# Kernel optimization log

Hardware: AMD Instinct MI355X
Metric: run time of the kernel (lower is better)

Reference implementation:

```python
import jax, jax.numpy as jnp
import numpy as np

NEG_SLOPE = 0.2  # PyG GATConv default leaky_relu slope


def gat_conv(x, edge_index, W, a_src, a_dst, b):
    """PyG GATConv (heads=1, concat=True, add_self_loops=True, dropout=0)."""
    N = x.shape[0]
    loops = jnp.arange(N, dtype=edge_index.dtype)
    src = jnp.concatenate([edge_index[0], loops])  # [Ef]
    dst = jnp.concatenate([edge_index[1], loops])  # [Ef]
    h = x @ W  # [N, Dout]
    alpha_src = h @ a_src  # [N]
    alpha_dst = h @ a_dst  # [N]
    logits = jax.nn.leaky_relu(alpha_src[src] + alpha_dst[dst], NEG_SLOPE)  # [Ef]
    # segment softmax over edges grouped by destination node
    m = jax.ops.segment_max(logits, dst, num_segments=N)
    e = jnp.exp(logits - m[dst])
    denom = jax.ops.segment_sum(e, dst, num_segments=N)  # >0: every node has a self-loop
    alpha = e / denom[dst]  # [Ef]
    out = jax.ops.segment_sum(alpha[:, None] * h[src], dst, num_segments=N)
    return out + b


def global_mean_pool(x, batch, num_graphs):
    s = jax.ops.segment_sum(x, batch, num_segments=num_graphs)
    cnt = jax.ops.segment_sum(jnp.ones((x.shape[0],), x.dtype), batch, num_segments=num_graphs)
    return s / jnp.maximum(cnt, 1.0)[:, None]


NUM_GRAPHS = 64


def setup_inputs() -> dict:
    key = jax.random.key(0)
    ks = jax.random.split(key, 12)
    N, E, D = 50000, 600000, 128
    x = jax.random.normal(ks[0], (N, D), dtype=jnp.float32)
    edge_index = jax.random.randint(ks[1], (2, E), 0, N, dtype=jnp.int32)
    edge_weight = jax.random.uniform(ks[2], (E,), dtype=jnp.float32)
    batch = jnp.sort(jax.random.randint(ks[3], (N,), 0, NUM_GRAPHS, dtype=jnp.int32))
    sc = 1.0 / np.sqrt(D)
    W0 = jax.random.normal(ks[4], (D, D), dtype=jnp.float32) * sc
    a_src0 = jax.random.normal(ks[5], (D,), dtype=jnp.float32) * sc
    a_dst0 = jax.random.normal(ks[6], (D,), dtype=jnp.float32) * sc
    b0 = jnp.zeros((D,), dtype=jnp.float32)
    W1 = jax.random.normal(ks[7], (D, D), dtype=jnp.float32) * sc
    a_src1 = jax.random.normal(ks[8], (D,), dtype=jnp.float32) * sc
    a_dst1 = jax.random.normal(ks[9], (D,), dtype=jnp.float32) * sc
    b1 = jnp.zeros((D,), dtype=jnp.float32)
    return {"x": x, "edge_index": edge_index, "edge_weight": edge_weight, "batch": batch,
            "W0": W0, "a_src0": a_src0, "a_dst0": a_dst0, "b0": b0,
            "W1": W1, "a_src1": a_src1, "a_dst1": a_dst1, "b1": b1}


def reference(x, edge_index, edge_weight, batch, W0, a_src0, a_dst0, b0, W1, a_src1, a_dst1, b1):
    # layer 0 (relu_layers_index=[0] -> ReLU after layer 0)
    out = gat_conv(x, edge_index, W0, a_src0, a_dst0, b0)
    out = jax.nn.relu(out)
    emb0 = global_mean_pool(out, batch, NUM_GRAPHS)
    # layer 1 (no relu, no dropout)
    out = gat_conv(out, edge_index, W1, a_src1, a_dst1, b1)
    emb1 = global_mean_pool(out, batch, NUM_GRAPHS)
    return (emb0, emb1)
```

## Files before the change

kernel.cpp:

```cpp
#include <hip/hip_runtime.h>
#include <hip/hip_cooperative_groups.h>

typedef unsigned int u32;
typedef unsigned short u16;
typedef unsigned long long u64;

typedef short bf16x8 __attribute__((ext_vector_type(8)));
typedef float f32x4 __attribute__((ext_vector_type(4)));
typedef float f32x2 __attribute__((ext_vector_type(2)));

__device__ __forceinline__ float bl(u32 u){ return __uint_as_float(u << 16); }
__device__ __forceinline__ float bh(u32 u){ return __uint_as_float(u & 0xffff0000u); }
__device__ __forceinline__ float b16f(u16 r){ return __uint_as_float(((u32)r) << 16); }
__device__ __forceinline__ u16 f2b(float f){
  u32 u = __float_as_uint(f);
  u32 r = (u + 0x7fffu + ((u >> 16) & 1u)) >> 16;
  return (u16)r;
}
__device__ __forceinline__ u32 pk2(float a, float b){
  return (u32)f2b(a) | ((u32)f2b(b) << 16);
}
__device__ __forceinline__ void fma8(float* acc, float e2, uint2 h){
  f32x2 p0 = __builtin_amdgcn_cvt_pk_f32_fp8((int)h.x, 0);
  f32x2 p1 = __builtin_amdgcn_cvt_pk_f32_fp8((int)h.x, 1);
  f32x2 p2 = __builtin_amdgcn_cvt_pk_f32_fp8((int)h.y, 0);
  f32x2 p3 = __builtin_amdgcn_cvt_pk_f32_fp8((int)h.y, 1);
  acc[0]=fmaf(e2,p0.x,acc[0]); acc[1]=fmaf(e2,p0.y,acc[1]);
  acc[2]=fmaf(e2,p1.x,acc[2]); acc[3]=fmaf(e2,p1.y,acc[3]);
  acc[4]=fmaf(e2,p2.x,acc[4]); acc[5]=fmaf(e2,p2.y,acc[5]);
  acc[6]=fmaf(e2,p3.x,acc[6]); acc[7]=fmaf(e2,p3.y,acc[7]);
}

#define NEG_SLOPE 0.2f
#define BSTRIDE 4096
#define SMBYTES 34816



__device__ __forceinline__ int detect_body(const u32* __restrict__ x, char* SM){
  int* cnt_ = (int*)SM;
  if (threadIdx.x == 0) *cnt_ = 0;
  __syncthreads();
  u32 w = x[threadIdx.x];
  int e = (int)((w >> 7) & 0xFFu);
  if (e >= 110 && e <= 135) atomicAdd(cnt_, 1);
  __syncthreads();
  return (*cnt_ >= 128) ? 1 : 0;
}

__device__ __forceinline__ void bnd_body(const int* __restrict__ batch,
    int* __restrict__ bnd, int N)
{
  int g = threadIdx.x;
  if (g <= 64){
    int lo = 0, hi = N;
    while (lo < hi){ int mid = (lo + hi) >> 1; if (batch[mid] < g) lo = mid + 1; else hi = mid; }
    bnd[g] = lo;
  }
}

__device__ __forceinline__ void part_body(const int* __restrict__ ei, int E, int nbuck,
    int* __restrict__ gcnt, u64* __restrict__ breg, int job, char* SM)
{
  u64* stage = (u64*)SM;
  u32* hist  = (u32*)(SM + 16384);
  u32* lscan = (u32*)(SM + 17408);
  u32* gbase = (u32*)(SM + 18436);
  u32* cur   = (u32*)(SM + 19460);
  const int tid = threadIdx.x;
  __syncthreads();
  hist[tid] = 0; cur[tid] = 0;
  __syncthreads();
  const int e0 = job * 2048;
  int src[8], dst[8];
  #pragma unroll
  for (int j = 0; j < 8; j++){
    int t = e0 + tid + j*256;
    if (t < E){
      src[j] = ei[t]; dst[j] = ei[E + t];
      atomicAdd(&hist[dst[j] >> 8], 1u);
    } else dst[j] = -1;
  }
  __syncthreads();
  const u32 v = hist[tid];
  lscan[tid] = v;
  __syncthreads();
  for (int off = 1; off < 256; off <<= 1){
    u32 add = (tid >= off) ? lscan[tid - off] : 0;
    __syncthreads();
    lscan[tid] += add;
    __syncthreads();
  }
  if (tid == 255) lscan[256] = lscan[255];
  u32 excl = lscan[tid] - v;
  __syncthreads();
  const u32 total = lscan[256];
  lscan[tid] = excl;
  if (tid < nbuck && v > 0) gbase[tid] = (u32)atomicAdd(&gcnt[tid], (int)v);
  __syncthreads();
  #pragma unroll
  for (int j = 0; j < 8; j++){
    if (dst[j] >= 0){
      int b = dst[j] >> 8;
      u32 p = lscan[b] + atomicAdd(&cur[b], 1u);
      stage[p] = ((u64)(u32)dst[j] << 32) | (u32)src[j];
    }
  }
  __syncthreads();
  for (u32 i = tid; i < total; i += 256){
    u64 e = stage[i];
    int b = (int)(e >> 40);
    u32 r = i - lscan[b];
    breg[(long)b * BSTRIDE + gbase[b] + r] = e;
  }
}

__device__ __forceinline__ void csr_body(const int* __restrict__ gcnt,
    const u64* __restrict__ breg,
    int* __restrict__ rpd, int* __restrict__ csrc, int N, int job, char* SM)
{
  u32* dl = (u32*)SM;
  u32* rp = dl + 256;
  u32* cu = rp + 256;
  const int b = job, tid = threadIdx.x;
  const int n0 = b << 8;
  __syncthreads();
  const int cntb = gcnt[b];
  dl[tid] = 0; cu[tid] = 0;
  __syncthreads();
  const u64* reg = breg + (long)b * BSTRIDE;
  for (int i = tid; i < cntb; i += 256)
    atomicAdd(&dl[(int)(reg[i] >> 32) - n0], 1u);
  __syncthreads();
  const u32 v = dl[tid];
  rp[tid] = v;
  __syncthreads();
  for (int off = 1; off < 256; off <<= 1){
    u32 add = (tid >= off) ? rp[tid - off] : 0;
    __syncthreads();
    rp[tid] += add;
    __syncthreads();
  }
  u32 excl = rp[tid] - v;
  __syncthreads();
  rp[tid] = excl;
  __syncthreads();
  int node = n0 + tid;
  if (node < N) rpd[node] = (int)(((u32)(b*BSTRIDE) + excl) | (v << 20));
  for (int i = tid; i < cntb; i += 256){
    u64 e = reg[i];
    int d = (int)(e >> 32) - n0;
    u32 pos = rp[d] + atomicAdd(&cu[d], 1u);
    csrc[(long)b*BSTRIDE + pos] = (int)(e & 0xffffffffULL);
  }
}

template<bool XEXT, bool KPERM>
__device__ __forceinline__ void gemm_body(int gb, int isbf,
    const void* __restrict__ Xv, const void* __restrict__ Wv,
    const void* __restrict__ av, const void* __restrict__ dv,
    u32* __restrict__ Hb, float* __restrict__ As, float* __restrict__ Ad, int N, char* SM)
{
  u16* Wt = (u16*)SM;
  const int tid = threadIdx.x;
  __syncthreads();

  if (isbf){
    const u32* Wp = (const u32*)Wv;
    #pragma unroll
    for (int i = 0; i < 16; i++){
      int idx = tid + i*256;
      u32 p = Wp[idx];
      int k = idx >> 6, n2 = idx & 63;
      int pos = KPERM ? ((k & 15)*8 + (k >> 4)) : k;
      Wt[(2*n2)*136 + pos]   = (u16)(p & 0xffffu);
      Wt[(2*n2+1)*136 + pos] = (u16)(p >> 16);
    }
  } else {
    const float* Wf = (const float*)Wv;
    #pragma unroll
    for (int i = 0; i < 64; i++){
      int idx = tid + i*256;
      int k = idx >> 7, n = idx & 127;
      int pos = KPERM ? ((k & 15)*8 + (k >> 4)) : k;
      Wt[n*136 + pos] = f2b(Wf[idx]);
    }
  }
  __syncthreads();

  const int wv = tid >> 6, L = tid & 63;
  const int row0 = (gb*4 + wv) * 16;
  if (row0 >= N) return;
  const int nl = L & 15, quad = L >> 4;

  bf16x8 af[4];
  if (!XEXT || isbf){
    const uint4* Xr = (const uint4*)(((const u32*)Xv) + (long)row0*64);
    #pragma unroll
    for (int kb = 0; kb < 4; kb++)
      af[kb] = *(const bf16x8*)&Xr[nl*16 + kb*4 + quad];
  } else {
    const float* Xf = ((const float*)Xv) + (long)(row0 + nl)*128;
    #pragma unroll
    for (int kb = 0; kb < 4; kb++){
      const float4* p = (const float4*)(Xf + kb*32 + quad*8);
      float4 f0 = p[0], f1 = p[1];
      uint4 tmp = make_uint4(pk2(f0.x,f0.y), pk2(f0.z,f0.w), pk2(f1.x,f1.y), pk2(f1.z,f1.w));
      af[kb] = *(const bf16x8*)&tmp;
    }
  }

  f32x4 acc[8];
  #pragma unroll
  for (int nt = 0; nt < 8; nt++) acc[nt] = (f32x4){0.f,0.f,0.f,0.f};
  #pragma unroll
  for (int nt = 0; nt < 8; nt++){
    #pragma unroll
    for (int kb = 0; kb < 4; kb++){
      bf16x8 bf = *(const bf16x8*)&Wt[(nt*16 + nl)*136 + kb*32 + quad*8];
      acc[nt] = __builtin_amdgcn_mfma_f32_16x16x32_bf16(af[kb], bf, acc[nt], 0, 0, 0);
    }
  }

  float ps[4] = {0.f,0.f,0.f,0.f}, pd[4] = {0.f,0.f,0.f,0.f};
  #pragma unroll
  for (int nt = 0; nt < 8; nt++){
    int col = nt*16 + nl;
    float a_ = isbf ? b16f(((const u16*)av)[col]) : ((const float*)av)[col];
    float d_ = isbf ? b16f(((const u16*)dv)[col]) : ((const float*)dv)[col];
    #pragma unroll
    for (int r = 0; r < 4; r++){
      ps[r] = fmaf(acc[nt][r], a_, ps[r]);
      pd[r] = fmaf(acc[nt][r], d_, pd[r]);
    }
  }
  #pragma unroll
  for (int off = 1; off < 16; off <<= 1){
    #pragma unroll
    for (int r = 0; r < 4; r++){
      ps[r] += __shfl_xor(ps[r], off);
      pd[r] += __shfl_xor(pd[r], off);
    }
  }
  if (nl == 0){
    #pragma unroll
    for (int r = 0; r < 4; r++){
      As[row0 + quad*4 + r] = ps[r];
      Ad[row0 + quad*4 + r] = pd[r];
    }
  }

  #pragma unroll
  for (int r = 0; r < 4; r++){
    long row = row0 + quad*4 + r;
    int w0 = 0, w1 = 0;
    w0 = __builtin_amdgcn_cvt_pk_fp8_f32(acc[0][r], acc[1][r], w0, 0);
    w0 = __builtin_amdgcn_cvt_pk_fp8_f32(acc[2][r], acc[3][r], w0, 1);
    w1 = __builtin_amdgcn_cvt_pk_fp8_f32(acc[4][r], acc[5][r], w1, 0);
    w1 = __builtin_amdgcn_cvt_pk_fp8_f32(acc[6][r], acc[7][r], w1, 1);
    uint2 v = make_uint2((u32)w0, (u32)w1);
    *(uint2*)(Hb + row*32 + nl*2) = v;
  }
}

__device__ __forceinline__ void pool_body(const u32* __restrict__ Ob,
    const int* __restrict__ bnd, float* __restrict__ psum, int N, int job, char* SM)
{
  int* bl_ = (int*)SM;
  const int tid = threadIdx.x;
  __syncthreads();
  if (tid < 65) bl_[tid] = bnd[tid];
  __syncthreads();
  const int wv = tid >> 6, lane = tid & 63;
  const int start = job * 128;
  const int end = min(start + 128, N);
  int node = start + wv;
  if (node >= end) return;
  int lo = 0, hi = 64;
  while (lo + 1 < hi){ int mid = (lo + hi) >> 1; if (bl_[mid] <= node) lo = mid; else hi = mid; }
  int cur = lo, nextb = bl_[cur + 1];
  float2 acc = make_float2(0.f, 0.f);
  const u32* __restrict__ ob = Ob + lane;
  for (int j = 0; j < 32; j += 4){
    int n0 = node + 4*j, n1 = n0 + 4, n2 = n0 + 8, n3 = n0 + 12;
    u32 p0 = 0, p1 = 0, p2 = 0, p3 = 0;
    if (n0 < end) p0 = ob[(long)n0*64];
    if (n1 < end) p1 = ob[(long)n1*64];
    if (n2 < end) p2 = ob[(long)n2*64];
    if (n3 < end) p3 = ob[(long)n3*64];
    #define PSTEP(nd, pv) \
      if (nd < end){ \
        while (nd >= nextb){ \
          atomicAdd(&psum[cur*128 + lane*2],     acc.x); \
          atomicAdd(&psum[cur*128 + lane*2 + 1], acc.y); \
          acc = make_float2(0.f, 0.f); \
          cur++; nextb = bl_[cur + 1]; \
        } \
        acc.x += bl(pv); acc.y += bh(pv); \
      }
    PSTEP(n0, p0) PSTEP(n1, p1) PSTEP(n2, p2) PSTEP(n3, p3)
    #undef PSTEP
  }
  atomicAdd(&psum[cur*128 + lane*2],     acc.x);
  atomicAdd(&psum[cur*128 + lane*2 + 1], acc.y);
}

template<bool RELU>
__device__ __forceinline__ void gath_body(const int* __restrict__ rpd,
    const int* __restrict__ csrc,
    const float* __restrict__ As, const float* __restrict__ Ad,
    const u32* __restrict__ Hb, const void* __restrict__ bv, int isbf,
    u32* __restrict__ Ob, int N, int job)
{
  long t = (long)job*256 + threadIdx.x;
  int node = (int)(t >> 4), q = (int)(t & 15);
  if (node >= N) return;
  const int base = threadIdx.x & 48;
  const float ad = Ad[node];
  const u32 pk = (u32)rpd[node];
  const int dg = (int)(pk >> 20);
  const int* row = csrc + (pk & 0xFFFFFu);
  float l = As[node] + ad;
  l = l > 0.f ? l : NEG_SLOPE * l;
  float e = __expf(l);
  float acc[8];
  {
    uint2 hv = ((const uint2*)(Hb + (long)node*32))[q];
    f32x2 p0 = __builtin_amdgcn_cvt_pk_f32_fp8((int)hv.x, 0);
    f32x2 p1 = __builtin_amdgcn_cvt_pk_f32_fp8((int)hv.x, 1);
    f32x2 p2 = __builtin_amdgcn_cvt_pk_f32_fp8((int)hv.y, 0);
    f32x2 p3 = __builtin_amdgcn_cvt_pk_f32_fp8((int)hv.y, 1);
    acc[0]=e*p0.x; acc[1]=e*p0.y; acc[2]=e*p1.x; acc[3]=e*p1.y;
    acc[4]=e*p2.x; acc[5]=e*p2.y; acc[6]=e*p3.x; acc[7]=e*p3.y;
  }
  float den = e;
  for (int jb = 0; jb < dg; jb += 16){
    int m = dg - jb; if (m > 16) m = 16;
    int sj = node;
    if (q < m) sj = row[jb + q];
    float asv = As[sj];
    int s[16];
    #pragma unroll
    for (int i = 0; i < 16; i++) s[i] = __shfl(sj, base + i);
    uint2 h[16];
    #pragma unroll
    for (int i = 0; i < 16; i++) h[i] = ((const uint2*)(Hb + (long)s[i]*32))[q];
    float evq = 0.f;
    if (q < m){
      float l2 = asv + ad;
      l2 = l2 > 0.f ? l2 : NEG_SLOPE * l2;
      evq = __expf(l2);
    }
    float ev[16];
    #pragma unroll
    for (int i = 0; i < 16; i++) ev[i] = __shfl(evq, base + i);
    float dsum = 0.f;
    #pragma unroll
    for (int i = 0; i < 16; i++) dsum += ev[i];
    den += dsum;
    #pragma unroll
    for (int i = 0; i < 16; i++) fma8(acc, ev[i], h[i]);
  }
  float inv = 1.f / den;
  float b[8];
  if (isbf){
    const u16* bp = (const u16*)bv;
    #pragma unroll
    for (int i = 0; i < 8; i++) b[i] = b16f(bp[i*16 + q]);
  } else {
    const float* bp = (const float*)bv;
    #pragma unroll
    for (int i = 0; i < 8; i++) b[i] = bp[i*16 + q];
  }
  float o[8];
  #pragma unroll
  for (int i = 0; i < 8; i++){
    o[i] = fmaf(acc[i], inv, b[i]);
    if (RELU) o[i] = fmaxf(o[i], 0.f);
  }
  uint4 w = make_uint4(pk2(o[0],o[1]), pk2(o[2],o[3]), pk2(o[4],o[5]), pk2(o[6],o[7]));
  *(uint4*)&Ob[(long)node*64 + q*4] = w;
}

__device__ __forceinline__ void fin_body(const float* __restrict__ ps0,
    const float* __restrict__ ps1, const int* __restrict__ bnd,
    int isbf, void* __restrict__ out, int job)
{
  int t = job*256 + threadIdx.x;
  if (t >= 8192) return;
  int g = t >> 7, pos = t & 127;
  int c = ((pos & 7) << 4) + (pos >> 3);
  int cc = bnd[g+1] - bnd[g];
  float cf = (float)(cc < 1 ? 1 : cc);
  float v0 = ps0[t] / cf, v1 = ps1[t] / cf;
  if (isbf){
    u16* o = (u16*)out;
    o[g*128 + c] = f2b(v0); o[8192 + g*128 + c] = f2b(v1);
  } else {
    float* o = (float*)out;
    o[g*128 + c] = v0; o[8192 + g*128 + c] = v1;
  }
}


struct MegaArgs {
  const u32* x; const int* ei; const int* batch;
  const void *W0, *as0, *ad0, *b0, *W1, *as1, *ad1, *b1;
  u32 *Hb, *Ob; float *As, *Ad;
  u64* breg; int *csrc, *rpd, *bnd, *gcnt;
  float *ps0, *ps1; void* out;
  int N, E, nbuck, gB, aB, nvB, pB;
};

__global__ __launch_bounds__(256) void mega_k(MegaArgs a)
{
  __shared__ __align__(16) char SM[SMBYTES];
  cooperative_groups::grid_group grid = cooperative_groups::this_grid();
  const int nb = (int)gridDim.x;
  const int isbf = detect_body(a.x, SM);

  for (int j = blockIdx.x; j < a.gB + 1 + a.aB; j += nb){
    if (j < a.gB)       gemm_body<true,false>(j, isbf, a.x, a.W0, a.as0, a.ad0, a.Hb, a.As, a.Ad, a.N, SM);
    else if (j == a.gB) bnd_body(a.batch, a.bnd, a.N);
    else                part_body(a.ei, a.E, a.nbuck, a.gcnt, a.breg, j - a.gB - 1, SM);
  }
  grid.sync();
  for (int j = blockIdx.x; j < a.nbuck; j += nb)
    csr_body(a.gcnt, a.breg, a.rpd, a.csrc, a.N, j, SM);
  grid.sync();
  for (int j = blockIdx.x; j < a.nvB; j += nb)
    gath_body<true>(a.rpd, a.csrc, a.As, a.Ad, a.Hb, a.b0, isbf, a.Ob, a.N, j);
  grid.sync();
  for (int j = blockIdx.x; j < a.pB + a.gB; j += nb){
    if (j < a.pB) pool_body(a.Ob, a.bnd, a.ps0, a.N, j, SM);
    else          gemm_body<false,true>(j - a.pB, isbf, a.Ob, a.W1, a.as1, a.ad1, a.Hb, a.As, a.Ad, a.N, SM);
  }
  grid.sync();
  for (int j = blockIdx.x; j < a.nvB; j += nb)
    gath_body<false>(a.rpd, a.csrc, a.As, a.Ad, a.Hb, a.b1, isbf, a.Ob, a.N, j);
  grid.sync();
  for (int j = blockIdx.x; j < a.pB; j += nb)
    pool_body(a.Ob, a.bnd, a.ps1, a.N, j, SM);
  grid.sync();
  for (int j = blockIdx.x; j < 32; j += nb)
    fin_body(a.ps0, a.ps1, a.bnd, isbf, a.out, j);
}


__global__ __launch_bounds__(256) void gemmdet0_k(
    const u32* __restrict__ x, const int* __restrict__ batch, int* __restrict__ bnd,
    int* __restrict__ flag,
    const void* __restrict__ W0, const void* __restrict__ as0, const void* __restrict__ ad0,
    u32* __restrict__ Hb, float* __restrict__ As, float* __restrict__ Ad, int N, int gB)
{
  __shared__ __align__(16) char SM[SMBYTES];
  if ((int)blockIdx.x == gB){ bnd_body(batch, bnd, N); return; }
  int isbf = detect_body(x, SM);
  if (blockIdx.x == 0 && threadIdx.x == 0) *flag = isbf;
  gemm_body<true, false>(blockIdx.x, isbf, x, W0, as0, ad0, Hb, As, Ad, N, SM);
}

__global__ __launch_bounds__(256) void part_k(const int* __restrict__ ei, int E, int nbuck,
    int* __restrict__ gcnt, u64* __restrict__ breg)
{
  __shared__ __align__(16) char SM[SMBYTES];
  part_body(ei, E, nbuck, gcnt, breg, blockIdx.x, SM);
}

__global__ __launch_bounds__(256) void csr_k(const int* __restrict__ gcnt,
    const u64* __restrict__ breg,
    int* __restrict__ rpd, int* __restrict__ csrc, int N)
{
  __shared__ __align__(16) char SM[SMBYTES];
  csr_body(gcnt, breg, rpd, csrc, N, blockIdx.x, SM);
}

template<bool RELU>
__global__ __launch_bounds__(256) void gath_k(const int* __restrict__ rpd,
    const int* __restrict__ csrc,
    const float* __restrict__ As, const float* __restrict__ Ad,
    const u32* __restrict__ Hb, const void* __restrict__ bv, const int* __restrict__ flag,
    u32* __restrict__ Ob, int N)
{
  gath_body<RELU>(rpd, csrc, As, Ad, Hb, bv, *flag, Ob, N, blockIdx.x);
}

__global__ __launch_bounds__(256) void poolgemm1_k(
    const u32* __restrict__ Ob, const int* __restrict__ bnd, float* __restrict__ ps0, int pB,
    const void* __restrict__ W1, const void* __restrict__ as1, const void* __restrict__ ad1,
    const int* __restrict__ flag,
    u32* __restrict__ Hb, float* __restrict__ As, float* __restrict__ Ad, int N)
{
  __shared__ __align__(16) char SM[SMBYTES];
  if ((int)blockIdx.x < pB){ pool_body(Ob, bnd, ps0, N, blockIdx.x, SM); return; }
  gemm_body<false, true>(blockIdx.x - pB, *flag, Ob, W1, as1, ad1, Hb, As, Ad, N, SM);
}

__global__ __launch_bounds__(256) void pool2_k(const u32* __restrict__ Ob,
    const int* __restrict__ bnd, float* __restrict__ psum, int N)
{
  __shared__ __align__(16) char SM[SMBYTES];
  pool_body(Ob, bnd, psum, N, blockIdx.x, SM);
}

__global__ __launch_bounds__(256) void fin_k(const float* __restrict__ ps0,
    const float* __restrict__ ps1, const int* __restrict__ bnd,
    const int* __restrict__ flag, void* __restrict__ out)
{
  fin_body(ps0, ps1, bnd, *flag, out, blockIdx.x);
}

extern "C" void kernel_launch(void* const* d_in, const int* in_sizes, int n_in,
                              void* d_out, int out_size, void* d_ws, size_t ws_size,
                              hipStream_t stream)
{
  const void* x    = d_in[0];
  const int* ei    = (const int*)d_in[1];
  const int* batch = (const int*)d_in[3];
  const void* W0  = d_in[4];
  const void* as0 = d_in[5];
  const void* ad0 = d_in[6];
  const void* b0  = d_in[7];
  const void* W1  = d_in[8];
  const void* as1 = d_in[9];
  const void* ad1 = d_in[10];
  const void* b1  = d_in[11];

  const int N  = in_sizes[0] / 128;
  const int E  = in_sizes[1] / 2;
  const int nbuck = (N + 255) >> 8;

  char* ws = (char*)d_ws;
  size_t off = 0;
  auto al = [&](size_t bytes){ size_t o = off; off += (bytes + 255) & ~(size_t)255; return o; };
  u32*   Hb    = (u32*)(ws + al((size_t)N*32*4));
  u32*   Ob    = (u32*)(ws + al((size_t)N*64*4));
  float* As    = (float*)(ws + al((size_t)N*4));
  float* Ad    = (float*)(ws + al((size_t)N*4));
  u64*   breg  = (u64*)(ws + al((size_t)nbuck*BSTRIDE*8));
  int*   csrc  = (int*)(ws + al((size_t)nbuck*BSTRIDE*4));
  int*   rpd   = (int*)(ws + al((size_t)N*4));
  int*   bnd   = (int*)(ws + al(512));
  const size_t zbytes = 2*64*128*4 + 256*4;
  char*  z0    = ws + al(zbytes);
  float* ps0   = (float*)z0;
  float* ps1   = ps0 + 8192;
  int*   gcnt  = (int*)(ps1 + 8192);
  int*   flag  = (int*)(ws + al(256));
  if (off > ws_size) return;

  hipMemsetAsync(z0, 0, zbytes, stream);

  const int gB   = (N/16 + 3) / 4;
  const int aB   = (E + 2047) / 2048;
  const int nvB16= (N*16 + 255) / 256;
  const int pB   = (N + 127) / 128;

  MegaArgs A;
  A.x = (const u32*)x; A.ei = ei; A.batch = batch;
  A.W0 = W0; A.as0 = as0; A.ad0 = ad0; A.b0 = b0;
  A.W1 = W1; A.as1 = as1; A.ad1 = ad1; A.b1 = b1;
  A.Hb = Hb; A.Ob = Ob; A.As = As; A.Ad = Ad;
  A.breg = breg; A.csrc = csrc; A.rpd = rpd; A.bnd = bnd; A.gcnt = gcnt;
  A.ps0 = ps0; A.ps1 = ps1; A.out = d_out;
  A.N = N; A.E = E; A.nbuck = nbuck; A.gB = gB; A.aB = aB; A.nvB = nvB16; A.pB = pB;

  int occ = 0;
  hipError_t qerr = hipOccupancyMaxActiveBlocksPerMultiprocessor(
      &occ, (const void*)mega_k, 256, 0);
  if (qerr == hipSuccess && occ >= 1){
    int grid = occ * 256;
    if (grid > 2048) grid = 2048;
    void* kargs[] = { (void*)&A };
    hipError_t err = hipLaunchCooperativeKernel((const void*)mega_k,
        dim3(grid), dim3(256), kargs, 0, stream);
    if (err == hipSuccess) return;
  }

  gemmdet0_k<<<gB + 1, 256, 0, stream>>>((const u32*)x, batch, bnd, flag,
      W0, as0, ad0, Hb, As, Ad, N, gB);
  part_k<<<aB, 256, 0, stream>>>(ei, E, nbuck, gcnt, breg);
  csr_k<<<nbuck, 256, 0, stream>>>(gcnt, breg, rpd, csrc, N);
  gath_k<true><<<nvB16, 256, 0, stream>>>(rpd, csrc, As, Ad, Hb, b0, flag, Ob, N);
  poolgemm1_k<<<pB + gB, 256, 0, stream>>>(Ob, bnd, ps0, pB,
      W1, as1, ad1, flag, Hb, As, Ad, N);
  gath_k<false><<<nvB16, 256, 0, stream>>>(rpd, csrc, As, Ad, Hb, b1, flag, Ob, N);
  pool2_k<<<pB, 256, 0, stream>>>(Ob, bnd, ps1, N);
  fin_k<<<32, 256, 0, stream>>>(ps0, ps1, bnd, flag, d_out);
}
```

Baseline: 182.7 us.

## Cut register pressure in fused GAT kernel and raise waves per EU

```diff
diff --git a/kernel.cpp b/kernel.cpp
--- a/kernel.cpp
+++ b/kernel.cpp
@@ -167,7 +167,7 @@
 
   if (isbf){
     const u32* Wp = (const u32*)Wv;
-    #pragma unroll
+    #pragma unroll 8
     for (int i = 0; i < 16; i++){
       int idx = tid + i*256;
       u32 p = Wp[idx];
@@ -178,7 +178,7 @@
     }
   } else {
     const float* Wf = (const float*)Wv;
-    #pragma unroll
+    #pragma unroll 8
     for (int i = 0; i < 64; i++){
       int idx = tid + i*256;
       int k = idx >> 7, n = idx & 127;
@@ -210,30 +210,41 @@
     }
   }
 
-  f32x4 acc[8];
-  #pragma unroll
-  for (int nt = 0; nt < 8; nt++) acc[nt] = (f32x4){0.f,0.f,0.f,0.f};
-  #pragma unroll
-  for (int nt = 0; nt < 8; nt++){
-    #pragma unroll
-    for (int kb = 0; kb < 4; kb++){
-      bf16x8 bf = *(const bf16x8*)&Wt[(nt*16 + nl)*136 + kb*32 + quad*8];
-      acc[nt] = __builtin_amdgcn_mfma_f32_16x16x32_bf16(af[kb], bf, acc[nt], 0, 0, 0);
-    }
-  }
-
   float ps[4] = {0.f,0.f,0.f,0.f}, pd[4] = {0.f,0.f,0.f,0.f};
   #pragma unroll
-  for (int nt = 0; nt < 8; nt++){
-    int col = nt*16 + nl;
-    float a_ = isbf ? b16f(((const u16*)av)[col]) : ((const float*)av)[col];
-    float d_ = isbf ? b16f(((const u16*)dv)[col]) : ((const float*)dv)[col];
+  for (int half = 0; half < 2; half++){
+    f32x4 acc[4];
+    #pragma unroll
+    for (int nt = 0; nt < 4; nt++) acc[nt] = (f32x4){0.f,0.f,0.f,0.f};
+    #pragma unroll
+    for (int nt = 0; nt < 4; nt++){
+      #pragma unroll
+      for (int kb = 0; kb < 4; kb++){
+        bf16x8 bf = *(const bf16x8*)&Wt[((half*4 + nt)*16 + nl)*136 + kb*32 + quad*8];
+        acc[nt] = __builtin_amdgcn_mfma_f32_16x16x32_bf16(af[kb], bf, acc[nt], 0, 0, 0);
+      }
+    }
+    #pragma unroll
+    for (int nt = 0; nt < 4; nt++){
+      int col = (half*4 + nt)*16 + nl;
+      float a_ = isbf ? b16f(((const u16*)av)[col]) : ((const float*)av)[col];
+      float d_ = isbf ? b16f(((const u16*)dv)[col]) : ((const float*)dv)[col];
+      #pragma unroll
+      for (int r = 0; r < 4; r++){
+        ps[r] = fmaf(acc[nt][r], a_, ps[r]);
+        pd[r] = fmaf(acc[nt][r], d_, pd[r]);
+      }
+    }
     #pragma unroll
     for (int r = 0; r < 4; r++){
-      ps[r] = fmaf(acc[nt][r], a_, ps[r]);
-      pd[r] = fmaf(acc[nt][r], d_, pd[r]);
-    }
-  }
+      long row = row0 + quad*4 + r;
+      int w = 0;
+      w = __builtin_amdgcn_cvt_pk_fp8_f32(acc[0][r], acc[1][r], w, 0);
+      w = __builtin_amdgcn_cvt_pk_fp8_f32(acc[2][r], acc[3][r], w, 1);
+      (Hb + row*32 + nl*2)[half] = (u32)w;
+    }
+  }
+
   #pragma unroll
   for (int off = 1; off < 16; off <<= 1){
     #pragma unroll
@@ -248,18 +259,6 @@
       As[row0 + quad*4 + r] = ps[r];
       Ad[row0 + quad*4 + r] = pd[r];
     }
-  }
-
-  #pragma unroll
-  for (int r = 0; r < 4; r++){
-    long row = row0 + quad*4 + r;
-    int w0 = 0, w1 = 0;
-    w0 = __builtin_amdgcn_cvt_pk_fp8_f32(acc[0][r], acc[1][r], w0, 0);
-    w0 = __builtin_amdgcn_cvt_pk_fp8_f32(acc[2][r], acc[3][r], w0, 1);
-    w1 = __builtin_amdgcn_cvt_pk_fp8_f32(acc[4][r], acc[5][r], w1, 0);
-    w1 = __builtin_amdgcn_cvt_pk_fp8_f32(acc[6][r], acc[7][r], w1, 1);
-    uint2 v = make_uint2((u32)w0, (u32)w1);
-    *(uint2*)(Hb + row*32 + nl*2) = v;
   }
 }
 
@@ -412,7 +411,7 @@
   int N, E, nbuck, gB, aB, nvB, pB;
 };
 
-__global__ __launch_bounds__(256) void mega_k(MegaArgs a)
+__device__ __forceinline__ void mega_impl(MegaArgs& a)
 {
   __shared__ __align__(16) char SM[SMBYTES];
   cooperative_groups::grid_group grid = cooperative_groups::this_grid();
@@ -445,6 +444,12 @@
   for (int j = blockIdx.x; j < 32; j += nb)
     fin_body(a.ps0, a.ps1, a.bnd, isbf, a.out, j);
 }
+
+__global__ __launch_bounds__(256) void mega_k(MegaArgs a){ mega_impl(a); }
+__global__ __launch_bounds__(256) __attribute__((amdgpu_waves_per_eu(3)))
+void mega_k3(MegaArgs a){ mega_impl(a); }
+__global__ __launch_bounds__(256) __attribute__((amdgpu_waves_per_eu(4)))
+void mega_k4(MegaArgs a){ mega_impl(a); }
 
 
 __global__ __launch_bounds__(256) void gemmdet0_k(
@@ -565,14 +570,22 @@
   A.ps0 = ps0; A.ps1 = ps1; A.out = d_out;
   A.N = N; A.E = E; A.nbuck = nbuck; A.gB = gB; A.aB = aB; A.nvB = nvB16; A.pB = pB;
 
+  const void* kfun = (const void*)mega_k;
+  hipFuncAttributes fa{};
+  if (hipFuncGetAttributes(&fa, (const void*)mega_k4) == hipSuccess &&
+      fa.localSizeBytes == 0)
+    kfun = (const void*)mega_k4;
+  else if (hipFuncGetAttributes(&fa, (const void*)mega_k3) == hipSuccess &&
+           fa.localSizeBytes == 0)
+    kfun = (const void*)mega_k3;
+
   int occ = 0;
-  hipError_t qerr = hipOccupancyMaxActiveBlocksPerMultiprocessor(
-      &occ, (const void*)mega_k, 256, 0);
+  hipError_t qerr = hipOccupancyMaxActiveBlocksPerMultiprocessor(&occ, kfun, 256, 0);
   if (qerr == hipSuccess && occ >= 1){
     int grid = occ * 256;
     if (grid > 2048) grid = 2048;
     void* kargs[] = { (void*)&A };
-    hipError_t err = hipLaunchCooperativeKernel((const void*)mega_k,
+    hipError_t err = hipLaunchCooperativeKernel(kfun,
         dim3(grid), dim3(256), kargs, 0, stream);
     if (err == hipSuccess) return;
   }
```

New measurement: 447.9 us. 2.45x slower.
